# Kernel optimization log

Measured on AMD Instinct MI355X. Metric: run time of the kernel, lower is better.

Reference implementation:

```python
import jax, jax.numpy as jnp
import numpy as np

MAXHD, MAXV, MINA, MAXA, DT = 100.0, 40.0, -6.0, 4.0, 0.1
NVEH, NT, IN_DIM, UNITS = 4096, 1024, 12, 20


def setup_inputs() -> dict:
    key = jax.random.key(0)
    ks = jax.random.split(key, 12)
    leadfol_inputs = jax.random.normal(ks[0], (NVEH, NT, IN_DIM), dtype=jnp.float32)
    init_state = jax.random.normal(ks[1], (NVEH, 2), dtype=jnp.float32)
    hidden_states = jnp.zeros((2, NVEH, UNITS), dtype=jnp.float32)
    s = 0.1
    return {
        "leadfol_inputs": leadfol_inputs,
        "init_state": init_state,
        "hidden_states": hidden_states,
        "kernel": s * jax.random.normal(ks[2], (IN_DIM, 4 * UNITS), dtype=jnp.float32),
        "rkernel": s * jax.random.normal(ks[3], (UNITS, 4 * UNITS), dtype=jnp.float32),
        "bias": jnp.zeros((4 * UNITS,), dtype=jnp.float32),
        "W2": s * jax.random.normal(ks[4], (UNITS, 10), dtype=jnp.float32),
        "b2": jnp.zeros((10,), dtype=jnp.float32),
        "Wlc": s * jax.random.normal(ks[5], (10, 3), dtype=jnp.float32),
        "blc": jnp.zeros((3,), dtype=jnp.float32),
        "W1": s * jax.random.normal(ks[6], (10, 1), dtype=jnp.float32),
        "b1": jnp.zeros((1,), dtype=jnp.float32),
    }


def reference(leadfol_inputs, init_state, hidden_states, kernel, rkernel, bias,
              W2, b2, Wlc, blc, W1, b1):
    # time-major for scan: (nt, nveh, 12)
    xs = jnp.transpose(leadfol_inputs, (1, 0, 2))
    pos0, spd0 = init_state[:, 0], init_state[:, 1]
    h0, c0 = hidden_states[0], hidden_states[1]

    def step(carry, x_t):
        pos, spd, h, c = carry
        lead_hd = (x_t[:, :3] - pos[:, None]) / MAXHD
        fol_hd = (pos[:, None] - x_t[:, 3:6]) / MAXHD
        spds = x_t[:, 6:] / MAXV
        inp = jnp.concatenate([lead_hd, fol_hd, spds], axis=1)  # (nveh, 12)
        inp = jnp.where(jnp.isnan(inp), jnp.ones_like(inp), inp)
        # Keras LSTMCell (inference, no dropout): gate order i, f, g, o
        z = inp @ kernel + h @ rkernel + bias
        i_g, f_g, g_g, o_g = jnp.split(z, 4, axis=1)
        c_new = jax.nn.sigmoid(f_g) * c + jax.nn.sigmoid(i_g) * jnp.tanh(g_g)
        h_new = jax.nn.sigmoid(o_g) * jnp.tanh(c_new)
        x2 = jax.nn.relu(h_new @ W2 + b2)          # (nveh, 10)
        lc = x2 @ Wlc + blc                          # (nveh, 3)
        acc_raw = (x2 @ W1 + b1)[:, 0]               # (nveh,)
        acc = (MAXA - MINA) * acc_raw + MINA
        pos_new = pos + DT * spd
        spd_new = spd + DT * acc
        return (pos_new, spd_new, h_new, c_new), (pos_new, lc)

    (pos_f, spd_f, h_f, c_f), (traj, lc_all) = jax.lax.scan(step, (pos0, spd0, h0, c0), xs)
    pred_traj = jnp.transpose(traj, (1, 0))            # (nveh, nt)
    pred_lc_action = jnp.transpose(lc_all, (1, 0, 2))  # (nveh, nt, 3)
    return pred_traj, pred_lc_action, spd_f, (h_f, c_f)
```

## Files before the change

kernel.cpp:

```cpp
#include <hip/hip_runtime.h>
#include <cstdint>

#define NVEH  4096
#define NT    1024
#define INW   12
#define UNITS 20

typedef float f32x2 __attribute__((ext_vector_type(2)));

#define PIN(v)  asm volatile("" : "+v"(v))

#define PKFMA_LO(acc, w, s2) \
    asm("v_pk_fma_f32 %0, %1, %2, %0 op_sel:[0,0,0] op_sel_hi:[1,0,1]" \
        : "+v"(acc) : "v"(w), "v"(s2))
#define PKFMA_HI(acc, w, s2) \
    asm("v_pk_fma_f32 %0, %1, %2, %0 op_sel:[0,1,0] op_sel_hi:[1,1,1]" \
        : "+v"(acc) : "v"(w), "v"(s2))
#define PKMUL_LO(dst, w, s2) \
    asm("v_pk_mul_f32 %0, %1, %2 op_sel:[0,0] op_sel_hi:[1,0]" \
        : "=v"(dst) : "v"(w), "v"(s2))
#define PKFMA(acc, a, b) \
    asm("v_pk_fma_f32 %0, %1, %2, %0" : "+v"(acc) : "v"(a), "v"(b))

__device__ __forceinline__ float fexp2(float x) { return __builtin_amdgcn_exp2f(x); }
__device__ __forceinline__ float frcp(float x)  { return __builtin_amdgcn_rcpf(x); }

__device__ __forceinline__ void gload_lds16(const float* g, float* l) {
    __builtin_amdgcn_global_load_lds(
        (const __attribute__((address_space(1))) unsigned int*)g,
        (__attribute__((address_space(3))) unsigned int*)l,
        16, 0, 0);
}

__global__ __attribute__((amdgpu_waves_per_eu(2, 2))) __launch_bounds__(64)
void rnncf_kernel(const float* __restrict__ x,
                  const float* __restrict__ init_state,
                  const float* __restrict__ hs,
                  const float* __restrict__ K,
                  const float* __restrict__ R,
                  const float* __restrict__ bias,
                  const float* __restrict__ W2,
                  const float* __restrict__ b2,
                  const float* __restrict__ Wlc,
                  const float* __restrict__ blc,
                  const float* __restrict__ W1,
                  const float* __restrict__ b1,
                  float* __restrict__ out)
{
    const int lane = threadIdx.x;
    const int grp  = lane / 20;
    const int sub  = lane % 20;
    const int veh  = blockIdx.x * 3 + grp;
    const bool active = (grp < 3) && (veh < NVEH);
    const int vs = active ? veh : 0;

    __shared__ __align__(16) float x_lds[8][4][12];
    __shared__ __align__(16) float h_lds[4][20];
    __shared__ __align__(16) float x2_lds[4][12];

    const float s01l = -1.4426950408889634f;
    const float s01h = -1.4426950408889634f;
    const float s23l =  2.8853900817779268f;
    const float s23h = -1.4426950408889634f;
    f32x2 K01[12], K23[12], R01[20], R23[20], bz01, bz23;
    bz01[0] = s01l * bias[sub];      bz01[1] = s01h * bias[20 + sub];
    bz23[0] = s23l * bias[40 + sub]; bz23[1] = s23h * bias[60 + sub];
#pragma unroll
    for (int k = 0; k < 12; ++k) {
        K01[k][0] = s01l * K[k * 80 + sub];      K01[k][1] = s01h * K[k * 80 + 20 + sub];
        K23[k][0] = s23l * K[k * 80 + 40 + sub]; K23[k][1] = s23h * K[k * 80 + 60 + sub];
    }
#pragma unroll
    for (int k = 0; k < 20; ++k) {
        R01[k][0] = s01l * R[k * 80 + sub];      R01[k][1] = s01h * R[k * 80 + 20 + sub];
        R23[k][0] = s23l * R[k * 80 + 40 + sub]; R23[k][1] = s23h * R[k * 80 + 60 + sub];
    }
    const int mh = (sub < 10) ? sub : 9;
    f32x2 W2p[10];
#pragma unroll
    for (int u = 0; u < 10; ++u) {
        W2p[u][0] = W2[(2 * u) * 10 + mh];
        W2p[u][1] = W2[(2 * u + 1) * 10 + mh];
    }
    float b2s = b2[mh];
    const int jl = (sub < 3) ? sub : 0;
    f32x2 Wlcp[5];
#pragma unroll
    for (int m = 0; m < 5; ++m) {
        Wlcp[m][0] = Wlc[(2 * m) * 3 + jl];
        Wlcp[m][1] = Wlc[(2 * m + 1) * 3 + jl];
    }
    float blcs = blc[jl];
    f32x2 W1p[5];
#pragma unroll
    for (int m = 0; m < 5; ++m) { W1p[m][0] = W1[2 * m]; W1p[m][1] = W1[2 * m + 1]; }
    PIN(bz01); PIN(bz23);
#pragma unroll
    for (int k = 0; k < 12; ++k) { PIN(K01[k]); PIN(K23[k]); }
#pragma unroll
    for (int k = 0; k < 20; ++k) { PIN(R01[k]); PIN(R23[k]); }
#pragma unroll
    for (int u = 0; u < 10; ++u) PIN(W2p[u]);
#pragma unroll
    for (int m = 0; m < 5; ++m) { PIN(Wlcp[m]); PIN(W1p[m]); }
    PIN(b2s); PIN(blcs);

    float pos = init_state[vs * 2 + 0];
    float spd = init_state[vs * 2 + 1];
    float c   = hs[(size_t)NVEH * UNITS + (size_t)vs * UNITS + sub];
    float hnew = hs[(size_t)vs * UNITS + sub];

    h_lds[grp][sub] = hnew;
    __builtin_amdgcn_wave_barrier();
    f32x2 hrp[10];
#pragma unroll
    for (int q = 0; q < 5; ++q) {
        float4 v = ((const float4*)&h_lds[grp][0])[q];
        hrp[2*q][0]   = v.x; hrp[2*q][1]   = v.y;
        hrp[2*q+1][0] = v.z; hrp[2*q+1][1] = v.w;
    }
    __builtin_amdgcn_wave_barrier();

    const bool stg = (lane < 9);
    int sveh = blockIdx.x * 3 + lane / 3;
    if (sveh > NVEH - 1) sveh = NVEH - 1;
    const float* sgp = x + (size_t)sveh * NT * INW + (lane % 3) * 4;

    if (stg) {
#pragma unroll
        for (int t0 = 0; t0 < 8; ++t0)
            gload_lds16(sgp + (size_t)t0 * INW, &x_lds[t0][0][0]);
    }

    float* trajp = out + (size_t)vs * NT;
    float* lcp   = out + (size_t)NVEH * NT + (size_t)vs * NT * 3;

    float xm = 0.0f;

    for (int tb = 0; tb < NT; tb += 4) {
        asm volatile("s_waitcnt vmcnt(4)" ::: "memory");

#pragma unroll
        for (int j = 0; j < 4; ++j) {
            const int t = tb + j;

            float4 u0 = ((const float4*)&x_lds[t & 7][grp][0])[0];
            float4 u1 = ((const float4*)&x_lds[t & 7][grp][0])[1];
            float4 u2 = ((const float4*)&x_lds[t & 7][grp][0])[2];
            f32x2 x2p[5];
            if (t > 0) {
#pragma unroll
                for (int q = 0; q < 5; ++q)
                    x2p[q] = ((const f32x2*)&x2_lds[grp][0])[q];
            }
            __builtin_amdgcn_wave_barrier();

            const float pp = pos * 0.01f;
            f32x2 inp2[6];
            inp2[0][0] = fmaf(u0.x,  0.01f, -pp); inp2[0][1] = fmaf(u0.y,  0.01f, -pp);
            inp2[1][0] = fmaf(u0.z,  0.01f, -pp); inp2[1][1] = fmaf(u0.w, -0.01f,  pp);
            inp2[2][0] = fmaf(u1.x, -0.01f,  pp); inp2[2][1] = fmaf(u1.y, -0.01f,  pp);
            inp2[3][0] = u1.z * 0.025f;           inp2[3][1] = u1.w * 0.025f;
            inp2[4][0] = u2.x * 0.025f;           inp2[4][1] = u2.y * 0.025f;
            inp2[5][0] = u2.z * 0.025f;           inp2[5][1] = u2.w * 0.025f;

            f32x2 zK01 = bz01, zK23 = bz23;
#pragma unroll
            for (int q = 0; q < 6; ++q) {
                PKFMA_LO(zK01, K01[2*q],   inp2[q]);
                PKFMA_LO(zK23, K23[2*q],   inp2[q]);
                PKFMA_HI(zK01, K01[2*q+1], inp2[q]);
                PKFMA_HI(zK23, K23[2*q+1], inp2[q]);
            }
            f32x2 zA01, zA23, zB01, zB23;
            PKMUL_LO(zA01, R01[0], hrp[0]);
            PKMUL_LO(zA23, R23[0], hrp[0]);
            PKFMA_HI(zA01, R01[1], hrp[0]);
            PKFMA_HI(zA23, R23[1], hrp[0]);
#pragma unroll
            for (int q = 1; q < 5; ++q) {
                PKFMA_LO(zA01, R01[2*q],   hrp[q]);
                PKFMA_LO(zA23, R23[2*q],   hrp[q]);
                PKFMA_HI(zA01, R01[2*q+1], hrp[q]);
                PKFMA_HI(zA23, R23[2*q+1], hrp[q]);
            }
            PKMUL_LO(zB01, R01[10], hrp[5]);
            PKMUL_LO(zB23, R23[10], hrp[5]);
            PKFMA_HI(zB01, R01[11], hrp[5]);
            PKFMA_HI(zB23, R23[11], hrp[5]);
#pragma unroll
            for (int q = 6; q < 10; ++q) {
                PKFMA_LO(zB01, R01[2*q],   hrp[q]);
                PKFMA_LO(zB23, R23[2*q],   hrp[q]);
                PKFMA_HI(zB01, R01[2*q+1], hrp[q]);
                PKFMA_HI(zB23, R23[2*q+1], hrp[q]);
            }
            f32x2 z01 = (zK01 + zA01) + zB01;
            f32x2 z23 = (zK23 + zA23) + zB23;

            if (t > 0) {
                f32x2 ac2; ac2[0] = b1[0]; ac2[1] = 0.0f;
#pragma unroll
                for (int m = 0; m < 5; ++m) PKFMA(ac2, x2p[m], W1p[m]);
                float accr = ac2[0] + ac2[1];
                spd = fmaf(0.1f, fmaf(10.0f, accr, -6.0f), spd);
                if (active && sub < 3) {
                    f32x2 lc2; lc2[0] = blcs; lc2[1] = 0.0f;
#pragma unroll
                    for (int m = 0; m < 5; ++m) PKFMA(lc2, x2p[m], Wlcp[m]);
                    lcp[(t - 1) * 3 + sub] = lc2[0] + lc2[1];
                }
            }

            float ig = frcp(1.0f + fexp2(z01[0]));
            float fg = frcp(1.0f + fexp2(z01[1]));
            float gg = 1.0f - 2.0f * frcp(fexp2(z23[0]) + 1.0f);
            float og = frcp(1.0f + fexp2(z23[1]));
            c = fmaf(fg, c, ig * gg);
            float th = 1.0f - 2.0f * frcp(fexp2(2.8853900817779268f * c) + 1.0f);
            hnew = og * th;

            float posn = fmaf(0.1f, spd, pos);
            if (active && sub == 0) trajp[t] = posn;
            pos = posn;

            h_lds[grp][sub] = hnew;
            __builtin_amdgcn_wave_barrier();
#pragma unroll
            for (int q = 0; q < 5; ++q) {
                float4 v = ((const float4*)&h_lds[grp][0])[q];
                hrp[2*q][0]   = v.x; hrp[2*q][1]   = v.y;
                hrp[2*q+1][0] = v.z; hrp[2*q+1][1] = v.w;
            }
            __builtin_amdgcn_wave_barrier();

            f32x2 xm2; xm2[0] = b2s; xm2[1] = 0.0f;
#pragma unroll
            for (int u = 0; u < 10; ++u) PKFMA(xm2, hrp[u], W2p[u]);
            xm = fmaxf(xm2[0] + xm2[1], 0.0f);
            if (sub < 10) x2_lds[grp][sub] = xm;
            __builtin_amdgcn_wave_barrier();
        }

        if (stg) {
#pragma unroll
            for (int j = 0; j < 4; ++j) {
                int tt = tb + 8 + j; if (tt > NT - 1) tt = NT - 1;
                gload_lds16(sgp + (size_t)tt * INW, &x_lds[(tb + j) & 7][0][0]);
            }
        }
    }

    {
        f32x2 x2p[5];
#pragma unroll
        for (int q = 0; q < 5; ++q)
            x2p[q] = ((const f32x2*)&x2_lds[grp][0])[q];
        f32x2 ac2; ac2[0] = b1[0]; ac2[1] = 0.0f;
#pragma unroll
        for (int m = 0; m < 5; ++m) PKFMA(ac2, x2p[m], W1p[m]);
        float accr = ac2[0] + ac2[1];
        spd = fmaf(0.1f, fmaf(10.0f, accr, -6.0f), spd);
        if (active && sub < 3) {
            f32x2 lc2; lc2[0] = blcs; lc2[1] = 0.0f;
#pragma unroll
            for (int m = 0; m < 5; ++m) PKFMA(lc2, x2p[m], Wlcp[m]);
            lcp[(NT - 1) * 3 + sub] = lc2[0] + lc2[1];
        }
    }

    if (active) {
        float* spdf = out + (size_t)NVEH * NT * 4;
        float* hf   = spdf + NVEH;
        float* cf   = hf + (size_t)NVEH * UNITS;
        if (sub == 0) spdf[veh] = spd;
        hf[(size_t)veh * UNITS + sub] = hnew;
        cf[(size_t)veh * UNITS + sub] = c;
    }
}

extern "C" void kernel_launch(void* const* d_in, const int* in_sizes, int n_in,
                              void* d_out, int out_size, void* d_ws, size_t ws_size,
                              hipStream_t stream) {
    const float* x    = (const float*)d_in[0];
    const float* st0  = (const float*)d_in[1];
    const float* hs   = (const float*)d_in[2];
    const float* K    = (const float*)d_in[3];
    const float* R    = (const float*)d_in[4];
    const float* bias = (const float*)d_in[5];
    const float* W2   = (const float*)d_in[6];
    const float* b2   = (const float*)d_in[7];
    const float* Wlc  = (const float*)d_in[8];
    const float* blc  = (const float*)d_in[9];
    const float* W1   = (const float*)d_in[10];
    const float* b1   = (const float*)d_in[11];
    float* out = (float*)d_out;

    dim3 grid((NVEH + 2) / 3);
    dim3 block(64);
    hipLaunchKernelGGL(rnncf_kernel, grid, block, 0, stream,
                       x, st0, hs, K, R, bias, W2, b2, Wlc, blc, W1, b1, out);
}
```

Measured before the change: 690.3 us.

## Fold input scaling into weights and software-pipeline LSTM step computations

Folds the input normalization constants into the input kernel weights and separates the position-dependent term into a precomputed kd vector, so the x-projection for step t+1 can be computed ahead of time. The recurrent h·R product and the next x projection are moved to the end of each step, just after h is produced, which shortens the dependency chain at the start of the next step. Several wave barriers are dropped and W1 is read from memory (likely scalar loads) instead of being held in registers. This risks relying on implicit ordering of LDS accesses within a wave and adds register pressure.

Result: no change. 690.3 us (+0.0%).

```diff
diff --git a/kernel.cpp b/kernel.cpp
--- a/kernel.cpp
+++ b/kernel.cpp
@@ -58,22 +58,35 @@
     __shared__ __align__(16) float h_lds[4][20];
     __shared__ __align__(16) float x2_lds[4][12];
 
-    const float s01l = -1.4426950408889634f;
-    const float s01h = -1.4426950408889634f;
-    const float s23l =  2.8853900817779268f;
-    const float s23h = -1.4426950408889634f;
-    f32x2 K01[12], K23[12], R01[20], R23[20], bz01, bz23;
-    bz01[0] = s01l * bias[sub];      bz01[1] = s01h * bias[20 + sub];
-    bz23[0] = s23l * bias[40 + sub]; bz23[1] = s23h * bias[60 + sub];
+    const float L2E = 1.4426950408889634f;
+    const float sI = -L2E, sF = -L2E, sG = 2.0f * L2E, sO = -L2E;
+    f32x2 K01[12], K23[12], R01[20], R23[20], bz01, bz23, kd01, kd23;
 #pragma unroll
     for (int k = 0; k < 12; ++k) {
-        K01[k][0] = s01l * K[k * 80 + sub];      K01[k][1] = s01h * K[k * 80 + 20 + sub];
-        K23[k][0] = s23l * K[k * 80 + 40 + sub]; K23[k][1] = s23h * K[k * 80 + 60 + sub];
-    }
+        float ck = (k < 3) ? 0.01f : (k < 6) ? -0.01f : 0.025f;
+        K01[k][0] = sI * ck * K[k * 80 + sub];
+        K01[k][1] = sF * ck * K[k * 80 + 20 + sub];
+        K23[k][0] = sG * ck * K[k * 80 + 40 + sub];
+        K23[k][1] = sO * ck * K[k * 80 + 60 + sub];
+    }
+    {
+        float aI = 0, aF = 0, aG = 0, aO = 0;
+        for (int k = 0; k < 6; ++k) {
+            float sgn = (k < 3) ? -0.01f : 0.01f;
+            aI += sgn * K[k * 80 + sub];
+            aF += sgn * K[k * 80 + 20 + sub];
+            aG += sgn * K[k * 80 + 40 + sub];
+            aO += sgn * K[k * 80 + 60 + sub];
+        }
+        kd01[0] = sI * aI; kd01[1] = sF * aF;
+        kd23[0] = sG * aG; kd23[1] = sO * aO;
+    }
+    bz01[0] = sI * bias[sub];      bz01[1] = sF * bias[20 + sub];
+    bz23[0] = sG * bias[40 + sub]; bz23[1] = sO * bias[60 + sub];
 #pragma unroll
     for (int k = 0; k < 20; ++k) {
-        R01[k][0] = s01l * R[k * 80 + sub];      R01[k][1] = s01h * R[k * 80 + 20 + sub];
-        R23[k][0] = s23l * R[k * 80 + 40 + sub]; R23[k][1] = s23h * R[k * 80 + 60 + sub];
+        R01[k][0] = sI * R[k * 80 + sub];      R01[k][1] = sF * R[k * 80 + 20 + sub];
+        R23[k][0] = sG * R[k * 80 + 40 + sub]; R23[k][1] = sO * R[k * 80 + 60 + sub];
     }
     const int mh = (sub < 10) ? sub : 9;
     f32x2 W2p[10];
@@ -91,10 +104,7 @@
         Wlcp[m][1] = Wlc[(2 * m + 1) * 3 + jl];
     }
     float blcs = blc[jl];
-    f32x2 W1p[5];
-#pragma unroll
-    for (int m = 0; m < 5; ++m) { W1p[m][0] = W1[2 * m]; W1p[m][1] = W1[2 * m + 1]; }
-    PIN(bz01); PIN(bz23);
+    PIN(bz01); PIN(bz23); PIN(kd01); PIN(kd23);
 #pragma unroll
     for (int k = 0; k < 12; ++k) { PIN(K01[k]); PIN(K23[k]); }
 #pragma unroll
@@ -102,7 +112,7 @@
 #pragma unroll
     for (int u = 0; u < 10; ++u) PIN(W2p[u]);
 #pragma unroll
-    for (int m = 0; m < 5; ++m) { PIN(Wlcp[m]); PIN(W1p[m]); }
+    for (int m = 0; m < 5; ++m) PIN(Wlcp[m]);
     PIN(b2s); PIN(blcs);
 
     float pos = init_state[vs * 2 + 0];
@@ -110,6 +120,16 @@
     float c   = hs[(size_t)NVEH * UNITS + (size_t)vs * UNITS + sub];
     float hnew = hs[(size_t)vs * UNITS + sub];
 
+    const bool stg = (lane < 9);
+    int sveh = blockIdx.x * 3 + lane / 3;
+    if (sveh > NVEH - 1) sveh = NVEH - 1;
+    const float* sgp = x + (size_t)sveh * NT * INW + (lane % 3) * 4;
+    if (stg) {
+#pragma unroll
+        for (int t0 = 0; t0 < 8; ++t0)
+            gload_lds16(sgp + (size_t)t0 * INW, &x_lds[t0][0][0]);
+    }
+
     h_lds[grp][sub] = hnew;
     __builtin_amdgcn_wave_barrier();
     f32x2 hrp[10];
@@ -121,88 +141,71 @@
     }
     __builtin_amdgcn_wave_barrier();
 
-    const bool stg = (lane < 9);
-    int sveh = blockIdx.x * 3 + lane / 3;
-    if (sveh > NVEH - 1) sveh = NVEH - 1;
-    const float* sgp = x + (size_t)sveh * NT * INW + (lane % 3) * 4;
-
-    if (stg) {
-#pragma unroll
-        for (int t0 = 0; t0 < 8; ++t0)
-            gload_lds16(sgp + (size_t)t0 * INW, &x_lds[t0][0][0]);
-    }
+    asm volatile("s_waitcnt vmcnt(7)" ::: "memory");
+    f32x2 zKx01, zKx23, zA01, zA23, zB01, zB23;
+    {
+        float4 u0 = ((const float4*)&x_lds[0][grp][0])[0];
+        float4 u1 = ((const float4*)&x_lds[0][grp][0])[1];
+        float4 u2 = ((const float4*)&x_lds[0][grp][0])[2];
+        f32x2 xp[6];
+        xp[0][0]=u0.x; xp[0][1]=u0.y; xp[1][0]=u0.z; xp[1][1]=u0.w;
+        xp[2][0]=u1.x; xp[2][1]=u1.y; xp[3][0]=u1.z; xp[3][1]=u1.w;
+        xp[4][0]=u2.x; xp[4][1]=u2.y; xp[5][0]=u2.z; xp[5][1]=u2.w;
+        zKx01 = bz01; zKx23 = bz23;
+#pragma unroll
+        for (int q = 0; q < 6; ++q) {
+            PKFMA_LO(zKx01, K01[2*q],   xp[q]);
+            PKFMA_LO(zKx23, K23[2*q],   xp[q]);
+            PKFMA_HI(zKx01, K01[2*q+1], xp[q]);
+            PKFMA_HI(zKx23, K23[2*q+1], xp[q]);
+        }
+    }
+    PKMUL_LO(zA01, R01[0], hrp[0]);
+    PKMUL_LO(zA23, R23[0], hrp[0]);
+    PKFMA_HI(zA01, R01[1], hrp[0]);
+    PKFMA_HI(zA23, R23[1], hrp[0]);
+#pragma unroll
+    for (int q = 1; q < 5; ++q) {
+        PKFMA_LO(zA01, R01[2*q],   hrp[q]);
+        PKFMA_LO(zA23, R23[2*q],   hrp[q]);
+        PKFMA_HI(zA01, R01[2*q+1], hrp[q]);
+        PKFMA_HI(zA23, R23[2*q+1], hrp[q]);
+    }
+    PKMUL_LO(zB01, R01[10], hrp[5]);
+    PKMUL_LO(zB23, R23[10], hrp[5]);
+    PKFMA_HI(zB01, R01[11], hrp[5]);
+    PKFMA_HI(zB23, R23[11], hrp[5]);
+#pragma unroll
+    for (int q = 6; q < 10; ++q) {
+        PKFMA_LO(zB01, R01[2*q],   hrp[q]);
+        PKFMA_LO(zB23, R23[2*q],   hrp[q]);
+        PKFMA_HI(zB01, R01[2*q+1], hrp[q]);
+        PKFMA_HI(zB23, R23[2*q+1], hrp[q]);
+    }
+
+    f32x2 x2p[5];
+#pragma unroll
+    for (int q = 0; q < 5; ++q) { x2p[q][0] = 0.0f; x2p[q][1] = 0.0f; }
+    f32x2 posp; posp[0] = pos; posp[1] = 0.0f;
 
     float* trajp = out + (size_t)vs * NT;
     float* lcp   = out + (size_t)NVEH * NT + (size_t)vs * NT * 3;
 
-    float xm = 0.0f;
-
     for (int tb = 0; tb < NT; tb += 4) {
-        asm volatile("s_waitcnt vmcnt(4)" ::: "memory");
+        asm volatile("s_waitcnt vmcnt(3)" ::: "memory");
 
 #pragma unroll
         for (int j = 0; j < 4; ++j) {
             const int t = tb + j;
 
-            float4 u0 = ((const float4*)&x_lds[t & 7][grp][0])[0];
-            float4 u1 = ((const float4*)&x_lds[t & 7][grp][0])[1];
-            float4 u2 = ((const float4*)&x_lds[t & 7][grp][0])[2];
-            f32x2 x2p[5];
             if (t > 0) {
-#pragma unroll
-                for (int q = 0; q < 5; ++q)
-                    x2p[q] = ((const f32x2*)&x2_lds[grp][0])[q];
-            }
-            __builtin_amdgcn_wave_barrier();
-
-            const float pp = pos * 0.01f;
-            f32x2 inp2[6];
-            inp2[0][0] = fmaf(u0.x,  0.01f, -pp); inp2[0][1] = fmaf(u0.y,  0.01f, -pp);
-            inp2[1][0] = fmaf(u0.z,  0.01f, -pp); inp2[1][1] = fmaf(u0.w, -0.01f,  pp);
-            inp2[2][0] = fmaf(u1.x, -0.01f,  pp); inp2[2][1] = fmaf(u1.y, -0.01f,  pp);
-            inp2[3][0] = u1.z * 0.025f;           inp2[3][1] = u1.w * 0.025f;
-            inp2[4][0] = u2.x * 0.025f;           inp2[4][1] = u2.y * 0.025f;
-            inp2[5][0] = u2.z * 0.025f;           inp2[5][1] = u2.w * 0.025f;
-
-            f32x2 zK01 = bz01, zK23 = bz23;
-#pragma unroll
-            for (int q = 0; q < 6; ++q) {
-                PKFMA_LO(zK01, K01[2*q],   inp2[q]);
-                PKFMA_LO(zK23, K23[2*q],   inp2[q]);
-                PKFMA_HI(zK01, K01[2*q+1], inp2[q]);
-                PKFMA_HI(zK23, K23[2*q+1], inp2[q]);
-            }
-            f32x2 zA01, zA23, zB01, zB23;
-            PKMUL_LO(zA01, R01[0], hrp[0]);
-            PKMUL_LO(zA23, R23[0], hrp[0]);
-            PKFMA_HI(zA01, R01[1], hrp[0]);
-            PKFMA_HI(zA23, R23[1], hrp[0]);
-#pragma unroll
-            for (int q = 1; q < 5; ++q) {
-                PKFMA_LO(zA01, R01[2*q],   hrp[q]);
-                PKFMA_LO(zA23, R23[2*q],   hrp[q]);
-                PKFMA_HI(zA01, R01[2*q+1], hrp[q]);
-                PKFMA_HI(zA23, R23[2*q+1], hrp[q]);
-            }
-            PKMUL_LO(zB01, R01[10], hrp[5]);
-            PKMUL_LO(zB23, R23[10], hrp[5]);
-            PKFMA_HI(zB01, R01[11], hrp[5]);
-            PKFMA_HI(zB23, R23[11], hrp[5]);
-#pragma unroll
-            for (int q = 6; q < 10; ++q) {
-                PKFMA_LO(zB01, R01[2*q],   hrp[q]);
-                PKFMA_LO(zB23, R23[2*q],   hrp[q]);
-                PKFMA_HI(zB01, R01[2*q+1], hrp[q]);
-                PKFMA_HI(zB23, R23[2*q+1], hrp[q]);
-            }
-            f32x2 z01 = (zK01 + zA01) + zB01;
-            f32x2 z23 = (zK23 + zA23) + zB23;
-
-            if (t > 0) {
-                f32x2 ac2; ac2[0] = b1[0]; ac2[1] = 0.0f;
-#pragma unroll
-                for (int m = 0; m < 5; ++m) PKFMA(ac2, x2p[m], W1p[m]);
-                float accr = ac2[0] + ac2[1];
+                float a0 = b1[0], a1 = 0.0f;
+#pragma unroll
+                for (int m = 0; m < 5; ++m) {
+                    a0 = fmaf(x2p[m][0], W1[2*m],   a0);
+                    a1 = fmaf(x2p[m][1], W1[2*m+1], a1);
+                }
+                float accr = a0 + a1;
                 spd = fmaf(0.1f, fmaf(10.0f, accr, -6.0f), spd);
                 if (active && sub < 3) {
                     f32x2 lc2; lc2[0] = blcs; lc2[1] = 0.0f;
@@ -211,6 +214,16 @@
                     lcp[(t - 1) * 3 + sub] = lc2[0] + lc2[1];
                 }
             }
+            const float pold = pos;
+            pos = fmaf(0.1f, spd, pold);
+            if (active && sub == 0) trajp[t] = pos;
+            posp[0] = pold;
+
+            f32x2 z01 = zKx01, z23 = zKx23;
+            PKFMA_LO(z01, kd01, posp);
+            PKFMA_LO(z23, kd23, posp);
+            z01 = (z01 + zA01) + zB01;
+            z23 = (z23 + zA23) + zB23;
 
             float ig = frcp(1.0f + fexp2(z01[0]));
             float fg = frcp(1.0f + fexp2(z01[1]));
@@ -220,26 +233,69 @@
             float th = 1.0f - 2.0f * frcp(fexp2(2.8853900817779268f * c) + 1.0f);
             hnew = og * th;
 
-            float posn = fmaf(0.1f, spd, pos);
-            if (active && sub == 0) trajp[t] = posn;
-            pos = posn;
-
             h_lds[grp][sub] = hnew;
-            __builtin_amdgcn_wave_barrier();
 #pragma unroll
             for (int q = 0; q < 5; ++q) {
                 float4 v = ((const float4*)&h_lds[grp][0])[q];
                 hrp[2*q][0]   = v.x; hrp[2*q][1]   = v.y;
                 hrp[2*q+1][0] = v.z; hrp[2*q+1][1] = v.w;
             }
-            __builtin_amdgcn_wave_barrier();
 
             f32x2 xm2; xm2[0] = b2s; xm2[1] = 0.0f;
 #pragma unroll
             for (int u = 0; u < 10; ++u) PKFMA(xm2, hrp[u], W2p[u]);
-            xm = fmaxf(xm2[0] + xm2[1], 0.0f);
+            float xm = fmaxf(xm2[0] + xm2[1], 0.0f);
             if (sub < 10) x2_lds[grp][sub] = xm;
-            __builtin_amdgcn_wave_barrier();
+            {
+                float4 a = ((const float4*)&x2_lds[grp][0])[0];
+                float4 b = ((const float4*)&x2_lds[grp][0])[1];
+                float2 e = *((const float2*)&x2_lds[grp][8]);
+                x2p[0][0]=a.x; x2p[0][1]=a.y; x2p[1][0]=a.z; x2p[1][1]=a.w;
+                x2p[2][0]=b.x; x2p[2][1]=b.y; x2p[3][0]=b.z; x2p[3][1]=b.w;
+                x2p[4][0]=e.x; x2p[4][1]=e.y;
+            }
+
+            PKMUL_LO(zA01, R01[0], hrp[0]);
+            PKMUL_LO(zA23, R23[0], hrp[0]);
+            PKFMA_HI(zA01, R01[1], hrp[0]);
+            PKFMA_HI(zA23, R23[1], hrp[0]);
+#pragma unroll
+            for (int q = 1; q < 5; ++q) {
+                PKFMA_LO(zA01, R01[2*q],   hrp[q]);
+                PKFMA_LO(zA23, R23[2*q],   hrp[q]);
+                PKFMA_HI(zA01, R01[2*q+1], hrp[q]);
+                PKFMA_HI(zA23, R23[2*q+1], hrp[q]);
+            }
+            PKMUL_LO(zB01, R01[10], hrp[5]);
+            PKMUL_LO(zB23, R23[10], hrp[5]);
+            PKFMA_HI(zB01, R01[11], hrp[5]);
+            PKFMA_HI(zB23, R23[11], hrp[5]);
+#pragma unroll
+            for (int q = 6; q < 10; ++q) {
+                PKFMA_LO(zB01, R01[2*q],   hrp[q]);
+                PKFMA_LO(zB23, R23[2*q],   hrp[q]);
+                PKFMA_HI(zB01, R01[2*q+1], hrp[q]);
+                PKFMA_HI(zB23, R23[2*q+1], hrp[q]);
+            }
+
+            {
+                int tn = t + 1; if (tn > NT - 1) tn = NT - 1;
+                float4 u0 = ((const float4*)&x_lds[tn & 7][grp][0])[0];
+                float4 u1 = ((const float4*)&x_lds[tn & 7][grp][0])[1];
+                float4 u2 = ((const float4*)&x_lds[tn & 7][grp][0])[2];
+                f32x2 xp[6];
+                xp[0][0]=u0.x; xp[0][1]=u0.y; xp[1][0]=u0.z; xp[1][1]=u0.w;
+                xp[2][0]=u1.x; xp[2][1]=u1.y; xp[3][0]=u1.z; xp[3][1]=u1.w;
+                xp[4][0]=u2.x; xp[4][1]=u2.y; xp[5][0]=u2.z; xp[5][1]=u2.w;
+                zKx01 = bz01; zKx23 = bz23;
+#pragma unroll
+                for (int q = 0; q < 6; ++q) {
+                    PKFMA_LO(zKx01, K01[2*q],   xp[q]);
+                    PKFMA_LO(zKx23, K23[2*q],   xp[q]);
+                    PKFMA_HI(zKx01, K01[2*q+1], xp[q]);
+                    PKFMA_HI(zKx23, K23[2*q+1], xp[q]);
+                }
+            }
         }
 
         if (stg) {
@@ -252,14 +308,13 @@
     }
 
     {
-        f32x2 x2p[5];
-#pragma unroll
-        for (int q = 0; q < 5; ++q)
-            x2p[q] = ((const f32x2*)&x2_lds[grp][0])[q];
-        f32x2 ac2; ac2[0] = b1[0]; ac2[1] = 0.0f;
-#pragma unroll
-        for (int m = 0; m < 5; ++m) PKFMA(ac2, x2p[m], W1p[m]);
-        float accr = ac2[0] + ac2[1];
+        float a0 = b1[0], a1 = 0.0f;
+#pragma unroll
+        for (int m = 0; m < 5; ++m) {
+            a0 = fmaf(x2p[m][0], W1[2*m],   a0);
+            a1 = fmaf(x2p[m][1], W1[2*m+1], a1);
+        }
+        float accr = a0 + a1;
         spd = fmaf(0.1f, fmaf(10.0f, accr, -6.0f), spd);
         if (active && sub < 3) {
             f32x2 lc2; lc2[0] = blcs; lc2[1] = 0.0f;
```

## Interleave two vehicle streams per wave and fold input scaling into weights

Applied to the files above, without the earlier changes.

Each wave now advances two independent sets of three vehicles, P and Q, interleaving their recurrence steps. The aim is to hide the latency of the serial LSTM dependency chain through instruction-level parallelism, with occupancy dropped to one wave per EU to free registers. The input normalisation and position offset are folded algebraically into precomputed K weights plus a kd vector, so the input dot product for step t+1 is computed early, off the critical path. Wlc and W1 move to LDS or scalar loads to save VGPRs. The grid is halved, which risks less latency hiding from fewer resident waves and register spills.

Measured after the change: 1.061 ms. 1.54x slower.

```diff
diff --git a/kernel.cpp b/kernel.cpp
--- a/kernel.cpp
+++ b/kernel.cpp
@@ -32,7 +32,7 @@
         16, 0, 0);
 }
 
-__global__ __attribute__((amdgpu_waves_per_eu(2, 2))) __launch_bounds__(64)
+__global__ __attribute__((amdgpu_waves_per_eu(1, 1))) __launch_bounds__(64)
 void rnncf_kernel(const float* __restrict__ x,
                   const float* __restrict__ init_state,
                   const float* __restrict__ hs,
@@ -50,30 +50,47 @@
     const int lane = threadIdx.x;
     const int grp  = lane / 20;
     const int sub  = lane % 20;
-    const int veh  = blockIdx.x * 3 + grp;
-    const bool active = (grp < 3) && (veh < NVEH);
-    const int vs = active ? veh : 0;
-
-    __shared__ __align__(16) float x_lds[8][4][12];
-    __shared__ __align__(16) float h_lds[4][20];
-    __shared__ __align__(16) float x2_lds[4][12];
-
-    const float s01l = -1.4426950408889634f;
-    const float s01h = -1.4426950408889634f;
-    const float s23l =  2.8853900817779268f;
-    const float s23h = -1.4426950408889634f;
-    f32x2 K01[12], K23[12], R01[20], R23[20], bz01, bz23;
-    bz01[0] = s01l * bias[sub];      bz01[1] = s01h * bias[20 + sub];
-    bz23[0] = s23l * bias[40 + sub]; bz23[1] = s23h * bias[60 + sub];
+    const int vehP = blockIdx.x * 6 + grp;
+    const int vehQ = vehP + 3;
+    const bool aP = (grp < 3) && (vehP < NVEH);
+    const bool aQ = (grp < 3) && (vehQ < NVEH);
+    const int vsP = (vehP < NVEH) ? vehP : NVEH - 1;
+    const int vsQ = (vehQ < NVEH) ? vehQ : NVEH - 1;
+
+    __shared__ __align__(16) float x_lds[8][6][12];
+    __shared__ __align__(16) float h_lds[2][4][20];
+    __shared__ __align__(16) float x2_lds[2][4][12];
+    __shared__ __align__(16) float wlcl[3][12];
+
+    const float L2E = 1.4426950408889634f;
+    const float sI = -L2E, sF = -L2E, sG = 2.0f * L2E, sO = -L2E;
+    f32x2 K01[12], K23[12], R01[20], R23[20], bz01, bz23, kd01, kd23;
 #pragma unroll
     for (int k = 0; k < 12; ++k) {
-        K01[k][0] = s01l * K[k * 80 + sub];      K01[k][1] = s01h * K[k * 80 + 20 + sub];
-        K23[k][0] = s23l * K[k * 80 + 40 + sub]; K23[k][1] = s23h * K[k * 80 + 60 + sub];
-    }
+        float ck = (k < 3) ? 0.01f : (k < 6) ? -0.01f : 0.025f;
+        K01[k][0] = sI * ck * K[k * 80 + sub];
+        K01[k][1] = sF * ck * K[k * 80 + 20 + sub];
+        K23[k][0] = sG * ck * K[k * 80 + 40 + sub];
+        K23[k][1] = sO * ck * K[k * 80 + 60 + sub];
+    }
+    {
+        float aI = 0, aF = 0, aG = 0, aO = 0;
+        for (int k = 0; k < 6; ++k) {
+            float sgn = (k < 3) ? -0.01f : 0.01f;
+            aI += sgn * K[k * 80 + sub];
+            aF += sgn * K[k * 80 + 20 + sub];
+            aG += sgn * K[k * 80 + 40 + sub];
+            aO += sgn * K[k * 80 + 60 + sub];
+        }
+        kd01[0] = sI * aI; kd01[1] = sF * aF;
+        kd23[0] = sG * aG; kd23[1] = sO * aO;
+    }
+    bz01[0] = sI * bias[sub];      bz01[1] = sF * bias[20 + sub];
+    bz23[0] = sG * bias[40 + sub]; bz23[1] = sO * bias[60 + sub];
 #pragma unroll
     for (int k = 0; k < 20; ++k) {
-        R01[k][0] = s01l * R[k * 80 + sub];      R01[k][1] = s01h * R[k * 80 + 20 + sub];
-        R23[k][0] = s23l * R[k * 80 + 40 + sub]; R23[k][1] = s23h * R[k * 80 + 60 + sub];
+        R01[k][0] = sI * R[k * 80 + sub];      R01[k][1] = sF * R[k * 80 + 20 + sub];
+        R23[k][0] = sG * R[k * 80 + 40 + sub]; R23[k][1] = sO * R[k * 80 + 60 + sub];
     }
     const int mh = (sub < 10) ? sub : 9;
     f32x2 W2p[10];
@@ -84,162 +101,198 @@
     }
     float b2s = b2[mh];
     const int jl = (sub < 3) ? sub : 0;
-    f32x2 Wlcp[5];
-#pragma unroll
-    for (int m = 0; m < 5; ++m) {
-        Wlcp[m][0] = Wlc[(2 * m) * 3 + jl];
-        Wlcp[m][1] = Wlc[(2 * m + 1) * 3 + jl];
-    }
     float blcs = blc[jl];
-    f32x2 W1p[5];
-#pragma unroll
-    for (int m = 0; m < 5; ++m) { W1p[m][0] = W1[2 * m]; W1p[m][1] = W1[2 * m + 1]; }
-    PIN(bz01); PIN(bz23);
+    PIN(bz01); PIN(bz23); PIN(kd01); PIN(kd23);
 #pragma unroll
     for (int k = 0; k < 12; ++k) { PIN(K01[k]); PIN(K23[k]); }
 #pragma unroll
     for (int k = 0; k < 20; ++k) { PIN(R01[k]); PIN(R23[k]); }
 #pragma unroll
     for (int u = 0; u < 10; ++u) PIN(W2p[u]);
-#pragma unroll
-    for (int m = 0; m < 5; ++m) { PIN(Wlcp[m]); PIN(W1p[m]); }
     PIN(b2s); PIN(blcs);
 
-    float pos = init_state[vs * 2 + 0];
-    float spd = init_state[vs * 2 + 1];
-    float c   = hs[(size_t)NVEH * UNITS + (size_t)vs * UNITS + sub];
-    float hnew = hs[(size_t)vs * UNITS + sub];
-
-    h_lds[grp][sub] = hnew;
+    for (int idx = lane; idx < 36; idx += 64) {
+        int j = idx / 12, m = idx % 12;
+        wlcl[j][m] = (m < 10) ? Wlc[m * 3 + j] : 0.0f;
+    }
+
+    float posP = init_state[vsP * 2 + 0], spdP = init_state[vsP * 2 + 1];
+    float posQ = init_state[vsQ * 2 + 0], spdQ = init_state[vsQ * 2 + 1];
+    float cP = hs[(size_t)NVEH * UNITS + (size_t)vsP * UNITS + sub];
+    float cQ = hs[(size_t)NVEH * UNITS + (size_t)vsQ * UNITS + sub];
+    float hnewP = hs[(size_t)vsP * UNITS + sub];
+    float hnewQ = hs[(size_t)vsQ * UNITS + sub];
+
+    h_lds[0][grp][sub] = hnewP;
+    h_lds[1][grp][sub] = hnewQ;
     __builtin_amdgcn_wave_barrier();
-    f32x2 hrp[10];
+    f32x2 hrpP[10], hrpQ[10];
 #pragma unroll
     for (int q = 0; q < 5; ++q) {
-        float4 v = ((const float4*)&h_lds[grp][0])[q];
-        hrp[2*q][0]   = v.x; hrp[2*q][1]   = v.y;
-        hrp[2*q+1][0] = v.z; hrp[2*q+1][1] = v.w;
+        float4 v = ((const float4*)&h_lds[0][grp][0])[q];
+        hrpP[2*q][0]   = v.x; hrpP[2*q][1]   = v.y;
+        hrpP[2*q+1][0] = v.z; hrpP[2*q+1][1] = v.w;
+        float4 w = ((const float4*)&h_lds[1][grp][0])[q];
+        hrpQ[2*q][0]   = w.x; hrpQ[2*q][1]   = w.y;
+        hrpQ[2*q+1][0] = w.z; hrpQ[2*q+1][1] = w.w;
     }
     __builtin_amdgcn_wave_barrier();
 
-    const bool stg = (lane < 9);
-    int sveh = blockIdx.x * 3 + lane / 3;
+    const bool stg = (lane < 18);
+    int sveh = blockIdx.x * 6 + lane / 3;
     if (sveh > NVEH - 1) sveh = NVEH - 1;
     const float* sgp = x + (size_t)sveh * NT * INW + (lane % 3) * 4;
-
     if (stg) {
 #pragma unroll
         for (int t0 = 0; t0 < 8; ++t0)
             gload_lds16(sgp + (size_t)t0 * INW, &x_lds[t0][0][0]);
     }
 
-    float* trajp = out + (size_t)vs * NT;
-    float* lcp   = out + (size_t)NVEH * NT + (size_t)vs * NT * 3;
-
-    float xm = 0.0f;
+#define KDOT(zk01, zk23, row, slot)                                          \
+    {                                                                        \
+        float4 u0 = ((const float4*)&x_lds[slot][row][0])[0];                \
+        float4 u1 = ((const float4*)&x_lds[slot][row][0])[1];                \
+        float4 u2 = ((const float4*)&x_lds[slot][row][0])[2];                \
+        f32x2 xp[6];                                                         \
+        xp[0][0]=u0.x; xp[0][1]=u0.y; xp[1][0]=u0.z; xp[1][1]=u0.w;          \
+        xp[2][0]=u1.x; xp[2][1]=u1.y; xp[3][0]=u1.z; xp[3][1]=u1.w;          \
+        xp[4][0]=u2.x; xp[4][1]=u2.y; xp[5][0]=u2.z; xp[5][1]=u2.w;          \
+        zk01 = bz01; zk23 = bz23;                                            \
+        _Pragma("unroll")                                                    \
+        for (int q_ = 0; q_ < 6; ++q_) {                                     \
+            PKFMA_LO(zk01, K01[2*q_],   xp[q_]);                             \
+            PKFMA_LO(zk23, K23[2*q_],   xp[q_]);                             \
+            PKFMA_HI(zk01, K01[2*q_+1], xp[q_]);                             \
+            PKFMA_HI(zk23, K23[2*q_+1], xp[q_]);                             \
+        }                                                                    \
+    }
+
+#define RDOTS(za01, za23, zb01, zb23, hrp)                                   \
+    PKMUL_LO(za01, R01[0], hrp[0]);                                          \
+    PKMUL_LO(za23, R23[0], hrp[0]);                                          \
+    PKFMA_HI(za01, R01[1], hrp[0]);                                          \
+    PKFMA_HI(za23, R23[1], hrp[0]);                                          \
+    _Pragma("unroll")                                                        \
+    for (int q_ = 1; q_ < 5; ++q_) {                                         \
+        PKFMA_LO(za01, R01[2*q_],   hrp[q_]);                                \
+        PKFMA_LO(za23, R23[2*q_],   hrp[q_]);                                \
+        PKFMA_HI(za01, R01[2*q_+1], hrp[q_]);                                \
+        PKFMA_HI(za23, R23[2*q_+1], hrp[q_]);                                \
+    }                                                                        \
+    PKMUL_LO(zb01, R01[10], hrp[5]);                                         \
+    PKMUL_LO(zb23, R23[10], hrp[5]);                                         \
+    PKFMA_HI(zb01, R01[11], hrp[5]);                                         \
+    PKFMA_HI(zb23, R23[11], hrp[5]);                                         \
+    _Pragma("unroll")                                                        \
+    for (int q_ = 6; q_ < 10; ++q_) {                                        \
+        PKFMA_LO(zb01, R01[2*q_],   hrp[q_]);                                \
+        PKFMA_LO(zb23, R23[2*q_],   hrp[q_]);                                \
+        PKFMA_HI(zb01, R01[2*q_+1], hrp[q_]);                                \
+        PKFMA_HI(zb23, R23[2*q_+1], hrp[q_]);                                \
+    }
+
+    asm volatile("s_waitcnt vmcnt(7)" ::: "memory");
+    f32x2 zKx01P, zKx23P, zA01P, zA23P, zB01P, zB23P;
+    f32x2 zKx01Q, zKx23Q, zA01Q, zA23Q, zB01Q, zB23Q;
+    KDOT(zKx01P, zKx23P, grp, 0);
+    KDOT(zKx01Q, zKx23Q, 3 + grp, 0);
+    RDOTS(zA01P, zA23P, zB01P, zB23P, hrpP);
+    RDOTS(zA01Q, zA23Q, zB01Q, zB23Q, hrpQ);
+
+    f32x2 x2pP[5], x2pQ[5];
+#pragma unroll
+    for (int q = 0; q < 5; ++q) {
+        x2pP[q][0] = 0.0f; x2pP[q][1] = 0.0f;
+        x2pQ[q][0] = 0.0f; x2pQ[q][1] = 0.0f;
+    }
+    f32x2 pospP, pospQ; pospP[1] = 0.0f; pospQ[1] = 0.0f;
+
+    float* trajpP = out + (size_t)vsP * NT;
+    float* trajpQ = out + (size_t)vsQ * NT;
+    float* lcpP   = out + (size_t)NVEH * NT + (size_t)vsP * NT * 3;
+    float* lcpQ   = out + (size_t)NVEH * NT + (size_t)vsQ * NT * 3;
+
+#define STEP_ABC(t, pos, spd, c, hnew, x2p, posp, zKx01, zKx23,              \
+                 zA01, zA23, zB01, zB23, act, lcp, trajp, bank)              \
+    {                                                                        \
+        if ((t) > 0) {                                                       \
+            float a0 = b1[0], a1 = 0.0f;                                     \
+            _Pragma("unroll")                                                \
+            for (int m_ = 0; m_ < 5; ++m_) {                                 \
+                a0 = fmaf(x2p[m_][0], W1[2*m_],   a0);                       \
+                a1 = fmaf(x2p[m_][1], W1[2*m_+1], a1);                       \
+            }                                                                \
+            spd = fmaf(0.1f, fmaf(10.0f, a0 + a1, -6.0f), spd);              \
+            if (act && sub < 3) {                                            \
+                f32x2 lc2; lc2[0] = blcs; lc2[1] = 0.0f;                     \
+                _Pragma("unroll")                                            \
+                for (int m_ = 0; m_ < 5; ++m_) {                             \
+                    f32x2 w_ = ((const f32x2*)&wlcl[jl][0])[m_];             \
+                    PKFMA(lc2, x2p[m_], w_);                                 \
+                }                                                            \
+                lcp[((t) - 1) * 3 + sub] = lc2[0] + lc2[1];                  \
+            }                                                                \
+        }                                                                    \
+        const float pold_ = pos;                                             \
+        pos = fmaf(0.1f, spd, pold_);                                        \
+        if (act && sub == 0) trajp[t] = pos;                                 \
+        posp[0] = pold_;                                                     \
+        f32x2 z01 = zKx01, z23 = zKx23;                                      \
+        PKFMA_LO(z01, kd01, posp);                                           \
+        PKFMA_LO(z23, kd23, posp);                                           \
+        z01 = (z01 + zA01) + zB01;                                           \
+        z23 = (z23 + zA23) + zB23;                                           \
+        float ig = frcp(1.0f + fexp2(z01[0]));                               \
+        float fg = frcp(1.0f + fexp2(z01[1]));                               \
+        float gg = 1.0f - 2.0f * frcp(fexp2(z23[0]) + 1.0f);                 \
+        float og = frcp(1.0f + fexp2(z23[1]));                               \
+        c = fmaf(fg, c, ig * gg);                                            \
+        float th = 1.0f - 2.0f * frcp(fexp2(2.8853900817779268f * c) + 1.0f);\
+        hnew = og * th;                                                      \
+        h_lds[bank][grp][sub] = hnew;                                        \
+    }
+
+#define STEP_DGEF(t, hrp, x2p, zKx01, zKx23, zA01, zA23, zB01, zB23,         \
+                  bank, xrow)                                                \
+    {                                                                        \
+        _Pragma("unroll")                                                    \
+        for (int q_ = 0; q_ < 5; ++q_) {                                     \
+            float4 v_ = ((const float4*)&h_lds[bank][grp][0])[q_];           \
+            hrp[2*q_][0]   = v_.x; hrp[2*q_][1]   = v_.y;                    \
+            hrp[2*q_+1][0] = v_.z; hrp[2*q_+1][1] = v_.w;                    \
+        }                                                                    \
+        int tn_ = (t) + 1; if (tn_ > NT - 1) tn_ = NT - 1;                   \
+        KDOT(zKx01, zKx23, xrow, tn_ & 7);                                   \
+        f32x2 xm2; xm2[0] = b2s; xm2[1] = 0.0f;                              \
+        _Pragma("unroll")                                                    \
+        for (int u_ = 0; u_ < 10; ++u_) PKFMA(xm2, hrp[u_], W2p[u_]);        \
+        float xm_ = fmaxf(xm2[0] + xm2[1], 0.0f);                            \
+        if (sub < 10) x2_lds[bank][grp][sub] = xm_;                          \
+        {                                                                    \
+            float4 a_ = ((const float4*)&x2_lds[bank][grp][0])[0];           \
+            float4 b_ = ((const float4*)&x2_lds[bank][grp][0])[1];           \
+            float2 e_ = *((const float2*)&x2_lds[bank][grp][8]);             \
+            x2p[0][0]=a_.x; x2p[0][1]=a_.y; x2p[1][0]=a_.z; x2p[1][1]=a_.w;  \
+            x2p[2][0]=b_.x; x2p[2][1]=b_.y; x2p[3][0]=b_.z; x2p[3][1]=b_.w;  \
+            x2p[4][0]=e_.x; x2p[4][1]=e_.y;                                  \
+        }                                                                    \
+        RDOTS(zA01, zA23, zB01, zB23, hrp);                                  \
+    }
 
     for (int tb = 0; tb < NT; tb += 4) {
-        asm volatile("s_waitcnt vmcnt(4)" ::: "memory");
+        asm volatile("s_waitcnt vmcnt(3)" ::: "memory");
 
 #pragma unroll
         for (int j = 0; j < 4; ++j) {
             const int t = tb + j;
-
-            float4 u0 = ((const float4*)&x_lds[t & 7][grp][0])[0];
-            float4 u1 = ((const float4*)&x_lds[t & 7][grp][0])[1];
-            float4 u2 = ((const float4*)&x_lds[t & 7][grp][0])[2];
-            f32x2 x2p[5];
-            if (t > 0) {
-#pragma unroll
-                for (int q = 0; q < 5; ++q)
-                    x2p[q] = ((const f32x2*)&x2_lds[grp][0])[q];
-            }
-            __builtin_amdgcn_wave_barrier();
-
-            const float pp = pos * 0.01f;
-            f32x2 inp2[6];
-            inp2[0][0] = fmaf(u0.x,  0.01f, -pp); inp2[0][1] = fmaf(u0.y,  0.01f, -pp);
-            inp2[1][0] = fmaf(u0.z,  0.01f, -pp); inp2[1][1] = fmaf(u0.w, -0.01f,  pp);
-            inp2[2][0] = fmaf(u1.x, -0.01f,  pp); inp2[2][1] = fmaf(u1.y, -0.01f,  pp);
-            inp2[3][0] = u1.z * 0.025f;           inp2[3][1] = u1.w * 0.025f;
-            inp2[4][0] = u2.x * 0.025f;           inp2[4][1] = u2.y * 0.025f;
-            inp2[5][0] = u2.z * 0.025f;           inp2[5][1] = u2.w * 0.025f;
-
-            f32x2 zK01 = bz01, zK23 = bz23;
-#pragma unroll
-            for (int q = 0; q < 6; ++q) {
-                PKFMA_LO(zK01, K01[2*q],   inp2[q]);
-                PKFMA_LO(zK23, K23[2*q],   inp2[q]);
-                PKFMA_HI(zK01, K01[2*q+1], inp2[q]);
-                PKFMA_HI(zK23, K23[2*q+1], inp2[q]);
-            }
-            f32x2 zA01, zA23, zB01, zB23;
-            PKMUL_LO(zA01, R01[0], hrp[0]);
-            PKMUL_LO(zA23, R23[0], hrp[0]);
-            PKFMA_HI(zA01, R01[1], hrp[0]);
-            PKFMA_HI(zA23, R23[1], hrp[0]);
-#pragma unroll
-            for (int q = 1; q < 5; ++q) {
-                PKFMA_LO(zA01, R01[2*q],   hrp[q]);
-                PKFMA_LO(zA23, R23[2*q],   hrp[q]);
-                PKFMA_HI(zA01, R01[2*q+1], hrp[q]);
-                PKFMA_HI(zA23, R23[2*q+1], hrp[q]);
-            }
-            PKMUL_LO(zB01, R01[10], hrp[5]);
-            PKMUL_LO(zB23, R23[10], hrp[5]);
-            PKFMA_HI(zB01, R01[11], hrp[5]);
-            PKFMA_HI(zB23, R23[11], hrp[5]);
-#pragma unroll
-            for (int q = 6; q < 10; ++q) {
-                PKFMA_LO(zB01, R01[2*q],   hrp[q]);
-                PKFMA_LO(zB23, R23[2*q],   hrp[q]);
-                PKFMA_HI(zB01, R01[2*q+1], hrp[q]);
-                PKFMA_HI(zB23, R23[2*q+1], hrp[q]);
-            }
-            f32x2 z01 = (zK01 + zA01) + zB01;
-            f32x2 z23 = (zK23 + zA23) + zB23;
-
-            if (t > 0) {
-                f32x2 ac2; ac2[0] = b1[0]; ac2[1] = 0.0f;
-#pragma unroll
-                for (int m = 0; m < 5; ++m) PKFMA(ac2, x2p[m], W1p[m]);
-                float accr = ac2[0] + ac2[1];
-                spd = fmaf(0.1f, fmaf(10.0f, accr, -6.0f), spd);
-                if (active && sub < 3) {
-                    f32x2 lc2; lc2[0] = blcs; lc2[1] = 0.0f;
-#pragma unroll
-                    for (int m = 0; m < 5; ++m) PKFMA(lc2, x2p[m], Wlcp[m]);
-                    lcp[(t - 1) * 3 + sub] = lc2[0] + lc2[1];
-                }
-            }
-
-            float ig = frcp(1.0f + fexp2(z01[0]));
-            float fg = frcp(1.0f + fexp2(z01[1]));
-            float gg = 1.0f - 2.0f * frcp(fexp2(z23[0]) + 1.0f);
-            float og = frcp(1.0f + fexp2(z23[1]));
-            c = fmaf(fg, c, ig * gg);
-            float th = 1.0f - 2.0f * frcp(fexp2(2.8853900817779268f * c) + 1.0f);
-            hnew = og * th;
-
-            float posn = fmaf(0.1f, spd, pos);
-            if (active && sub == 0) trajp[t] = posn;
-            pos = posn;
-
-            h_lds[grp][sub] = hnew;
-            __builtin_amdgcn_wave_barrier();
-#pragma unroll
-            for (int q = 0; q < 5; ++q) {
-                float4 v = ((const float4*)&h_lds[grp][0])[q];
-                hrp[2*q][0]   = v.x; hrp[2*q][1]   = v.y;
-                hrp[2*q+1][0] = v.z; hrp[2*q+1][1] = v.w;
-            }
-            __builtin_amdgcn_wave_barrier();
-
-            f32x2 xm2; xm2[0] = b2s; xm2[1] = 0.0f;
-#pragma unroll
-            for (int u = 0; u < 10; ++u) PKFMA(xm2, hrp[u], W2p[u]);
-            xm = fmaxf(xm2[0] + xm2[1], 0.0f);
-            if (sub < 10) x2_lds[grp][sub] = xm;
-            __builtin_amdgcn_wave_barrier();
+            STEP_ABC(t, posP, spdP, cP, hnewP, x2pP, pospP, zKx01P, zKx23P,
+                     zA01P, zA23P, zB01P, zB23P, aP, lcpP, trajpP, 0);
+            STEP_ABC(t, posQ, spdQ, cQ, hnewQ, x2pQ, pospQ, zKx01Q, zKx23Q,
+                     zA01Q, zA23Q, zB01Q, zB23Q, aQ, lcpQ, trajpQ, 1);
+            STEP_DGEF(t, hrpP, x2pP, zKx01P, zKx23P,
+                      zA01P, zA23P, zB01P, zB23P, 0, grp);
+            STEP_DGEF(t, hrpQ, x2pQ, zKx01Q, zKx23Q,
+                      zA01Q, zA23Q, zB01Q, zB23Q, 1, 3 + grp);
         }
 
         if (stg) {
@@ -251,31 +304,42 @@
         }
     }
 
+#define EPI(x2p, spd, act, lcp)                                              \
+    {                                                                        \
+        float a0 = b1[0], a1 = 0.0f;                                         \
+        _Pragma("unroll")                                                    \
+        for (int m_ = 0; m_ < 5; ++m_) {                                     \
+            a0 = fmaf(x2p[m_][0], W1[2*m_],   a0);                           \
+            a1 = fmaf(x2p[m_][1], W1[2*m_+1], a1);                           \
+        }                                                                    \
+        spd = fmaf(0.1f, fmaf(10.0f, a0 + a1, -6.0f), spd);                  \
+        if (act && sub < 3) {                                                \
+            f32x2 lc2; lc2[0] = blcs; lc2[1] = 0.0f;                         \
+            _Pragma("unroll")                                                \
+            for (int m_ = 0; m_ < 5; ++m_) {                                 \
+                f32x2 w_ = ((const f32x2*)&wlcl[jl][0])[m_];                 \
+                PKFMA(lc2, x2p[m_], w_);                                     \
+            }                                                                \
+            lcp[(NT - 1) * 3 + sub] = lc2[0] + lc2[1];                       \
+        }                                                                    \
+    }
+    EPI(x2pP, spdP, aP, lcpP);
+    EPI(x2pQ, spdQ, aQ, lcpQ);
+
     {
-        f32x2 x2p[5];
-#pragma unroll
-        for (int q = 0; q < 5; ++q)
-            x2p[q] = ((const f32x2*)&x2_lds[grp][0])[q];
-        f32x2 ac2; ac2[0] = b1[0]; ac2[1] = 0.0f;
-#pragma unroll
-        for (int m = 0; m < 5; ++m) PKFMA(ac2, x2p[m], W1p[m]);
-        float accr = ac2[0] + ac2[1];
-        spd = fmaf(0.1f, fmaf(10.0f, accr, -6.0f), spd);
-        if (active && sub < 3) {
-            f32x2 lc2; lc2[0] = blcs; lc2[1] = 0.0f;
-#pragma unroll
-            for (int m = 0; m < 5; ++m) PKFMA(lc2, x2p[m], Wlcp[m]);
-            lcp[(NT - 1) * 3 + sub] = lc2[0] + lc2[1];
-        }
-    }
-
-    if (active) {
         float* spdf = out + (size_t)NVEH * NT * 4;
         float* hf   = spdf + NVEH;
         float* cf   = hf + (size_t)NVEH * UNITS;
-        if (sub == 0) spdf[veh] = spd;
-        hf[(size_t)veh * UNITS + sub] = hnew;
-        cf[(size_t)veh * UNITS + sub] = c;
+        if (aP) {
+            if (sub == 0) spdf[vehP] = spdP;
+            hf[(size_t)vehP * UNITS + sub] = hnewP;
+            cf[(size_t)vehP * UNITS + sub] = cP;
+        }
+        if (aQ) {
+            if (sub == 0) spdf[vehQ] = spdQ;
+            hf[(size_t)vehQ * UNITS + sub] = hnewQ;
+            cf[(size_t)vehQ * UNITS + sub] = cQ;
+        }
     }
 }
 
@@ -296,7 +360,7 @@
     const float* b1   = (const float*)d_in[11];
     float* out = (float*)d_out;
 
-    dim3 grid((NVEH + 2) / 3);
+    dim3 grid((NVEH + 5) / 6);
     dim3 block(64);
     hipLaunchKernelGGL(rnncf_kernel, grid, block, 0, stream,
                        x, st0, hs, K, R, bias, W2, b2, Wlc, blc, W1, b1, out);
```
